# Performance work log

Hardware: AMD Instinct MI355X
Metric: run time of the kernel (lower is better)

## Reference

```python
import jax, jax.numpy as jnp
import numpy as np


def setup_inputs() -> dict:
    key = jax.random.key(0)
    ks = jax.random.split(key, 12)
    B, C, H, W = 8, 512, 48, 48
    HW = H * W
    inp = {
        'key': jax.random.normal(ks[0], (B, C, H, W), dtype=jnp.float32),
        'sds': jax.random.uniform(ks[1], (B, HW, H, W), dtype=jnp.float32),
        'global_bg': jax.random.normal(ks[2], (B, HW, C), dtype=jnp.float32),
        'global_fg': jax.random.normal(ks[3], (B, HW, C), dtype=jnp.float32),
        'local_bg': jax.random.normal(ks[4], (B, HW, C), dtype=jnp.float32),
        'local_fg': jax.random.normal(ks[5], (B, HW, C), dtype=jnp.float32),
        'overall_bg': jax.random.normal(ks[6], (B, 1, C), dtype=jnp.float32),
        'overall_fg': jax.random.normal(ks[7], (B, 1, C), dtype=jnp.float32),
        'short_bg': jax.random.normal(ks[8], (B, 1, C), dtype=jnp.float32),
        'short_fg': jax.random.normal(ks[9], (B, 1, C), dtype=jnp.float32),
        'long_bg': jax.random.normal(ks[10], (B, 1, C), dtype=jnp.float32),
        'long_fg': jax.random.normal(ks[11], (B, 1, C), dtype=jnp.float32),
    }
    return inp


def reference(key, sds, global_bg, global_fg, local_bg, local_fg,
              overall_bg, overall_fg, short_bg, short_fg, long_bg, long_fg):
    B, C, H, W = key.shape
    HW = H * W
    k = key.reshape(B, C, HW)                 # [B, C, HW]
    mask = sds.reshape(B, HW, HW)             # [B, HW(mem), HW(query)]

    def fine_max(bank, m=None):
        # bank: [B, HW, C]; score: [B, HW(mem), HW(query)]
        s = jnp.einsum('bmc,bcn->bmn', bank, k)
        if m is not None:
            s = s * m
        return jnp.max(s, axis=1).reshape(B, 1, H, W)

    def coarse(bank):
        # bank: [B, 1, C]
        return jnp.einsum('boc,bcn->bon', bank, k).reshape(B, 1, H, W)

    global_score = jnp.concatenate([fine_max(global_bg), fine_max(global_fg)], axis=1)
    local_score = jnp.concatenate([fine_max(local_bg, mask), fine_max(local_fg, mask)], axis=1)
    fine_score = jnp.concatenate([global_score, local_score], axis=1)

    coarse_score = jnp.concatenate([
        coarse(overall_bg), coarse(overall_fg),
        coarse(short_bg), coarse(short_fg),
        coarse(long_bg), coarse(long_fg),
    ], axis=1)

    matching_score = jnp.concatenate([fine_score, coarse_score], axis=1)  # [B, 10, H, W]
    return matching_score
```

## Files before the change

### kernel.cpp

```cpp
#include <hip/hip_runtime.h>

#define B_   8
#define C_   512
#define HW_  2304
#define BM   128
#define BN   128
#define BKQ  32
#define NKS  (C_ / BKQ)
#define NT_  (HW_ / BN)
#define MT_PER_BLOCK 3
#define MCHUNKS 6

typedef __bf16 bf16x8 __attribute__((ext_vector_type(8)));
typedef float  f32x4  __attribute__((ext_vector_type(4)));

__device__ __forceinline__ unsigned short f2bf(float f) {
  unsigned int u = __float_as_uint(f);
  u += 0x7FFF + ((u >> 16) & 1);
  return (unsigned short)(u >> 16);
}

__device__ __forceinline__ void gload_lds16(const void* g, void* l) {
  __builtin_amdgcn_global_load_lds(
      (const __attribute__((address_space(1))) unsigned int*)g,
      (__attribute__((address_space(3))) unsigned int*)l, 16, 0, 0);
}

__global__ void zero_out(float* __restrict__ out, int n) {
  int i = blockIdx.x * 256 + threadIdx.x;
  if (i < n) out[i] = 0.0f;
}

__global__ void transpose_coarse(const float* __restrict__ key,
                                 const float* __restrict__ v0, const float* __restrict__ v1,
                                 const float* __restrict__ v2, const float* __restrict__ v3,
                                 const float* __restrict__ v4, const float* __restrict__ v5,
                                 unsigned short* __restrict__ keyT,
                                 float* __restrict__ out) {
  __shared__ float tile[32][33];
  __shared__ float red2[6][8][32];
  int b  = blockIdx.z;
  int n0 = blockIdx.x * 32;
  int c0 = blockIdx.y * 32;
  int tx = threadIdx.x;
  int ty = threadIdx.y;
#pragma unroll
  for (int i = 0; i < 4; i++) {
    int c = c0 + ty + i * 8;
    tile[ty + i * 8][tx] = key[(size_t)b * C_ * HW_ + (size_t)c * HW_ + n0 + tx];
  }
  __syncthreads();
#pragma unroll
  for (int i = 0; i < 4; i++) {
    int n = n0 + ty + i * 8;
    keyT[(size_t)b * HW_ * C_ + (size_t)n * C_ + c0 + tx] = f2bf(tile[tx][ty + i * 8]);
  }
  float s[6] = {0.f, 0.f, 0.f, 0.f, 0.f, 0.f};
#pragma unroll
  for (int i = 0; i < 4; i++) {
    int cr = ty * 4 + i;
    int c  = c0 + cr;
    float kv = tile[cr][tx];
    s[0] += v0[b * C_ + c] * kv;
    s[1] += v1[b * C_ + c] * kv;
    s[2] += v2[b * C_ + c] * kv;
    s[3] += v3[b * C_ + c] * kv;
    s[4] += v4[b * C_ + c] * kv;
    s[5] += v5[b * C_ + c] * kv;
  }
#pragma unroll
  for (int j = 0; j < 6; j++) red2[j][ty][tx] = s[j];
  __syncthreads();
  if (ty < 6) {
    float a = 0.f;
#pragma unroll
    for (int k = 0; k < 8; k++) a += red2[ty][k][tx];
    atomicAdd(&out[((size_t)b * 10 + 4 + ty) * HW_ + n0 + tx], a);
  }
}

__global__ void convert_banks(const float* __restrict__ b0, const float* __restrict__ b1,
                              const float* __restrict__ b2, const float* __restrict__ b3,
                              unsigned short* __restrict__ out) {
  const size_t per = (size_t)B_ * HW_ * C_;
  int g = blockIdx.y;
  const float* src = (g == 0) ? b0 : (g == 1) ? b1 : (g == 2) ? b2 : b3;
  size_t i = ((size_t)blockIdx.x * blockDim.x + threadIdx.x) * 4;
  float4 v = *(const float4*)(src + i);
  ushort4 o;
  o.x = f2bf(v.x); o.y = f2bf(v.y); o.z = f2bf(v.z); o.w = f2bf(v.w);
  *(ushort4*)(out + g * per + i) = o;
}

__global__ __launch_bounds__(256, 3) void fine_kernel(
    const unsigned short* __restrict__ keyT,
    const unsigned short* __restrict__ banks,
    const float* __restrict__ sds,
    float* __restrict__ pmax) {
  int lin = blockIdx.x;
  int b   = lin & 7;
  int ix  = lin >> 3;
  int gp  = (ix >= 108) ? 1 : 0;
  int w   = ix - gp * 108;
  int mc  = w / NT_;
  int nt  = w % NT_;
  int n0  = nt * BN;

  __shared__ __align__(16) unsigned short sbuf[2][3][BM * BKQ];
  __shared__ float red[4 * BN];

  int t    = threadIdx.x;
  int wave = t >> 6;
  int lane = t & 63;
  int quad = lane >> 4;
  int l15  = lane & 15;
  int wm   = (wave & 1) * 64;
  int wn   = (wave >> 1) * 64;

  int ksub = (lane & 3) ^ ((lane >> 3) & 3);
  int swo  = (quad ^ ((l15 >> 1) & 3)) * 8;

  const unsigned short* bank0 = banks + ((size_t)(2 * gp) * B_ + b) * (size_t)HW_ * C_;
  const unsigned short* bank1 = banks + ((size_t)(2 * gp + 1) * B_ + b) * (size_t)HW_ * C_;
  const unsigned short* keyb  = keyT + (size_t)b * HW_ * C_;
  const float* maskb = sds + (size_t)b * HW_ * HW_;
  const bool masked = (gp == 1);

  auto STAGE = [&](int buf, int m0s, int kc) {
    unsigned short* A0d = &sbuf[buf][0][0];
    unsigned short* A1d = &sbuf[buf][1][0];
    unsigned short* Bd  = &sbuf[buf][2][0];
#pragma unroll
    for (int j = 0; j < 2; j++) {
      int rbase = j * 64 + wave * 16;
      size_t go = (size_t)(rbase + (lane >> 2)) * C_ + (size_t)kc * BKQ + ksub * 8;
      gload_lds16(bank0 + (size_t)m0s * C_ + go, &A0d[rbase * BKQ]);
      gload_lds16(bank1 + (size_t)m0s * C_ + go, &A1d[rbase * BKQ]);
      gload_lds16(keyb  + (size_t)n0  * C_ + go, &Bd [rbase * BKQ]);
    }
  };

  float rm0[4], rm1[4];
#pragma unroll
  for (int i = 0; i < 4; i++) { rm0[i] = -3.4e38f; rm1[i] = -3.4e38f; }

  int cur = 0;
  STAGE(0, mc * MT_PER_BLOCK * BM, 0);

  for (int mi = 0; mi < MT_PER_BLOCK; mi++) {
    int m0 = (mc * MT_PER_BLOCK + mi) * BM;
    f32x4 acc0[4][4], acc1[4][4];
#pragma unroll
    for (int i = 0; i < 4; i++)
#pragma unroll
      for (int j = 0; j < 4; j++)
#pragma unroll
        for (int e = 0; e < 4; e++) { acc0[i][j][e] = 0.0f; acc1[i][j][e] = 0.0f; }

    for (int kc = 0; kc < NKS; kc++) {
      __syncthreads();
      if (kc + 1 < NKS)                STAGE(cur ^ 1, m0, kc + 1);
      else if (mi + 1 < MT_PER_BLOCK)  STAGE(cur ^ 1, m0 + BM, 0);

      const unsigned short* A0s = &sbuf[cur][0][0];
      const unsigned short* A1s = &sbuf[cur][1][0];
      const unsigned short* Bs  = &sbuf[cur][2][0];
      bf16x8 a0[4], a1[4], bb[4];
#pragma unroll
      for (int ms = 0; ms < 4; ms++) {
        a0[ms] = *(const bf16x8*)(&A0s[(wm + ms * 16 + l15) * BKQ + swo]);
        a1[ms] = *(const bf16x8*)(&A1s[(wm + ms * 16 + l15) * BKQ + swo]);
      }
#pragma unroll
      for (int ns = 0; ns < 4; ns++)
        bb[ns] = *(const bf16x8*)(&Bs[(wn + ns * 16 + l15) * BKQ + swo]);
#pragma unroll
      for (int ms = 0; ms < 4; ms++)
#pragma unroll
        for (int ns = 0; ns < 4; ns++) {
          acc0[ms][ns] = __builtin_amdgcn_mfma_f32_16x16x32_bf16(
              a0[ms], bb[ns], acc0[ms][ns], 0, 0, 0);
          acc1[ms][ns] = __builtin_amdgcn_mfma_f32_16x16x32_bf16(
              a1[ms], bb[ns], acc1[ms][ns], 0, 0, 0);
        }
      cur ^= 1;
    }

#pragma unroll
    for (int ms = 0; ms < 4; ms++) {
#pragma unroll
      for (int ns = 0; ns < 4; ns++) {
        int n = n0 + wn + ns * 16 + l15;
#pragma unroll
        for (int r = 0; r < 4; r++) {
          int m = m0 + wm + ms * 16 + quad * 4 + r;
          float s0 = acc0[ms][ns][r];
          float s1 = acc1[ms][ns][r];
          if (masked) {
            float w_ = maskb[(size_t)m * HW_ + n];
            s0 *= w_; s1 *= w_;
          }
          rm0[ns] = fmaxf(rm0[ns], s0);
          rm1[ns] = fmaxf(rm1[ns], s1);
        }
      }
    }
  }

#pragma unroll
  for (int ns = 0; ns < 4; ns++) {
    float v = rm0[ns];
    v = fmaxf(v, __shfl_xor(v, 16, 64));
    v = fmaxf(v, __shfl_xor(v, 32, 64));
    rm0[ns] = v;
    float u = rm1[ns];
    u = fmaxf(u, __shfl_xor(u, 16, 64));
    u = fmaxf(u, __shfl_xor(u, 32, 64));
    rm1[ns] = u;
  }
  if (lane < 16) {
#pragma unroll
    for (int ns = 0; ns < 4; ns++) {
      red[(wave & 1) * BN + wn + ns * 16 + l15]           = rm0[ns];
      red[2 * BN + (wave & 1) * BN + wn + ns * 16 + l15]  = rm1[ns];
    }
  }
  __syncthreads();
  if (t < BN) {
    float vv0 = fmaxf(red[t], red[BN + t]);
    float vv1 = fmaxf(red[2 * BN + t], red[3 * BN + t]);
    pmax[(((size_t)mc * B_ + b) * 4 + 2 * gp)     * HW_ + n0 + t] = vv0;
    pmax[(((size_t)mc * B_ + b) * 4 + 2 * gp + 1) * HW_ + n0 + t] = vv1;
  }
}

__global__ void fine_combine(const float* __restrict__ pmax, float* __restrict__ out) {
  int i = blockIdx.x * 256 + threadIdx.x;
  if (i >= B_ * 4 * HW_) return;
  int n = i % HW_;
  int g = (i / HW_) % 4;
  int b = i / (HW_ * 4);
  float v = -3.4e38f;
#pragma unroll
  for (int mc = 0; mc < MCHUNKS; mc++)
    v = fmaxf(v, pmax[(((size_t)mc * B_ + b) * 4 + g) * HW_ + n]);
  out[((size_t)b * 10 + g) * HW_ + n] = v;
}

extern "C" void kernel_launch(void* const* d_in, const int* in_sizes, int n_in,
                              void* d_out, int out_size, void* d_ws, size_t ws_size,
                              hipStream_t stream) {
  const float* key  = (const float*)d_in[0];
  const float* sds  = (const float*)d_in[1];
  const float* gbg  = (const float*)d_in[2];
  const float* gfg  = (const float*)d_in[3];
  const float* lbg  = (const float*)d_in[4];
  const float* lfg  = (const float*)d_in[5];
  const float* obg  = (const float*)d_in[6];
  const float* ofg  = (const float*)d_in[7];
  const float* sbg  = (const float*)d_in[8];
  const float* sfg  = (const float*)d_in[9];
  const float* lobg = (const float*)d_in[10];
  const float* lofg = (const float*)d_in[11];
  float* out = (float*)d_out;

  unsigned short* keyT  = (unsigned short*)d_ws;
  unsigned short* banks = keyT + (size_t)B_ * HW_ * C_;
  float* pmax = (float*)(banks + (size_t)4 * B_ * HW_ * C_);

  zero_out<<<(out_size + 255) / 256, 256, 0, stream>>>(out, out_size);
  convert_banks<<<dim3((B_ * HW_ * C_) / (4 * 256), 4), 256, 0, stream>>>(gbg, gfg, lbg, lfg, banks);
  transpose_coarse<<<dim3(HW_ / 32, C_ / 32, B_), dim3(32, 8), 0, stream>>>(
      key, obg, ofg, sbg, sfg, lobg, lofg, keyT, out);
  fine_kernel<<<dim3(NT_ * MCHUNKS * 2 * B_), 256, 0, stream>>>(keyT, banks, sds, pmax);
  fine_combine<<<(B_ * 4 * HW_ + 255) / 256, 256, 0, stream>>>(pmax, out);
}
```

Before: 734.2 us.

## Deepen global-to-LDS prefetch to two stages with explicit waitcnt and barriers

```diff
diff --git a/kernel.cpp b/kernel.cpp
--- a/kernel.cpp
+++ b/kernel.cpp
@@ -10,6 +10,7 @@
 #define NT_  (HW_ / BN)
 #define MT_PER_BLOCK 3
 #define MCHUNKS 6
+#define NSTEPS (MT_PER_BLOCK * NKS)
 
 typedef __bf16 bf16x8 __attribute__((ext_vector_type(8)));
 typedef float  f32x4  __attribute__((ext_vector_type(4)));
@@ -126,10 +127,13 @@
   const float* maskb = sds + (size_t)b * HW_ * HW_;
   const bool masked = (gp == 1);
 
-  auto STAGE = [&](int buf, int m0s, int kc) {
-    unsigned short* A0d = &sbuf[buf][0][0];
-    unsigned short* A1d = &sbuf[buf][1][0];
-    unsigned short* Bd  = &sbuf[buf][2][0];
+  auto STAGE = [&](int P, int s) {
+    int mi  = s >> 4;
+    int kc  = s & 15;
+    int m0s = (mc * MT_PER_BLOCK + mi) * BM;
+    unsigned short* A0d = &sbuf[P][0][0];
+    unsigned short* A1d = &sbuf[P][1][0];
+    unsigned short* Bd  = &sbuf[P][2][0];
 #pragma unroll
     for (int j = 0; j < 2; j++) {
       int rbase = j * 64 + wave * 16;
@@ -144,48 +148,58 @@
 #pragma unroll
   for (int i = 0; i < 4; i++) { rm0[i] = -3.4e38f; rm1[i] = -3.4e38f; }
 
-  int cur = 0;
-  STAGE(0, mc * MT_PER_BLOCK * BM, 0);
+  f32x4 acc0[4][4], acc1[4][4];
+
+#define KSTEP(P, MI, KC)                                                       \
+  do {                                                                         \
+    int s_ = (MI) * 16 + (KC);                                                 \
+    if (s_ < NSTEPS - 2) asm volatile("s_waitcnt vmcnt(6)" ::: "memory");      \
+    else                 asm volatile("s_waitcnt vmcnt(0)" ::: "memory");      \
+    __builtin_amdgcn_s_barrier();                     \
+    __builtin_amdgcn_sched_barrier(0);                                         \
+    const unsigned short* A0s = &sbuf[P][0][0];                                \
+    const unsigned short* A1s = &sbuf[P][1][0];                                \
+    const unsigned short* Bs  = &sbuf[P][2][0];                                \
+    bf16x8 a0[4], a1[4], bb[4];                                                \
+    _Pragma("unroll") for (int ms = 0; ms < 4; ms++) {                         \
+      a0[ms] = *(const bf16x8*)(&A0s[(wm + ms * 16 + l15) * BKQ + swo]);       \
+      a1[ms] = *(const bf16x8*)(&A1s[(wm + ms * 16 + l15) * BKQ + swo]);       \
+    }                                                                          \
+    _Pragma("unroll") for (int ns = 0; ns < 4; ns++)                           \
+      bb[ns] = *(const bf16x8*)(&Bs[(wn + ns * 16 + l15) * BKQ + swo]);        \
+    asm volatile("s_waitcnt lgkmcnt(0)" ::: "memory");                         \
+    __builtin_amdgcn_sched_barrier(0);                                         \
+    __builtin_amdgcn_s_barrier();                \
+    __builtin_amdgcn_sched_barrier(0);                                         \
+    if (s_ + 2 < NSTEPS) STAGE(P, s_ + 2);       \
+    __builtin_amdgcn_s_setprio(1);                                             \
+    _Pragma("unroll") for (int ms = 0; ms < 4; ms++)                           \
+      _Pragma("unroll") for (int ns = 0; ns < 4; ns++) {                       \
+        acc0[ms][ns] = __builtin_amdgcn_mfma_f32_16x16x32_bf16(                \
+            a0[ms], bb[ns], acc0[ms][ns], 0, 0, 0);                            \
+        acc1[ms][ns] = __builtin_amdgcn_mfma_f32_16x16x32_bf16(                \
+            a1[ms], bb[ns], acc1[ms][ns], 0, 0, 0);                            \
+      }                                                                        \
+    __builtin_amdgcn_s_setprio(0);                                             \
+  } while (0)
+
+  STAGE(0, 0);
+  STAGE(1, 1);
 
   for (int mi = 0; mi < MT_PER_BLOCK; mi++) {
+#pragma unroll
+    for (int i = 0; i < 4; i++)
+#pragma unroll
+      for (int j = 0; j < 4; j++)
+#pragma unroll
+        for (int e = 0; e < 4; e++) { acc0[i][j][e] = 0.0f; acc1[i][j][e] = 0.0f; }
+
+    for (int kc2 = 0; kc2 < NKS; kc2 += 2) {
+      KSTEP(0, mi, kc2);
+      KSTEP(1, mi, kc2 + 1);
+    }
+
     int m0 = (mc * MT_PER_BLOCK + mi) * BM;
-    f32x4 acc0[4][4], acc1[4][4];
-#pragma unroll
-    for (int i = 0; i < 4; i++)
-#pragma unroll
-      for (int j = 0; j < 4; j++)
-#pragma unroll
-        for (int e = 0; e < 4; e++) { acc0[i][j][e] = 0.0f; acc1[i][j][e] = 0.0f; }
-
-    for (int kc = 0; kc < NKS; kc++) {
-      __syncthreads();
-      if (kc + 1 < NKS)                STAGE(cur ^ 1, m0, kc + 1);
-      else if (mi + 1 < MT_PER_BLOCK)  STAGE(cur ^ 1, m0 + BM, 0);
-
-      const unsigned short* A0s = &sbuf[cur][0][0];
-      const unsigned short* A1s = &sbuf[cur][1][0];
-      const unsigned short* Bs  = &sbuf[cur][2][0];
-      bf16x8 a0[4], a1[4], bb[4];
-#pragma unroll
-      for (int ms = 0; ms < 4; ms++) {
-        a0[ms] = *(const bf16x8*)(&A0s[(wm + ms * 16 + l15) * BKQ + swo]);
-        a1[ms] = *(const bf16x8*)(&A1s[(wm + ms * 16 + l15) * BKQ + swo]);
-      }
-#pragma unroll
-      for (int ns = 0; ns < 4; ns++)
-        bb[ns] = *(const bf16x8*)(&Bs[(wn + ns * 16 + l15) * BKQ + swo]);
-#pragma unroll
-      for (int ms = 0; ms < 4; ms++)
-#pragma unroll
-        for (int ns = 0; ns < 4; ns++) {
-          acc0[ms][ns] = __builtin_amdgcn_mfma_f32_16x16x32_bf16(
-              a0[ms], bb[ns], acc0[ms][ns], 0, 0, 0);
-          acc1[ms][ns] = __builtin_amdgcn_mfma_f32_16x16x32_bf16(
-              a1[ms], bb[ns], acc1[ms][ns], 0, 0, 0);
-        }
-      cur ^= 1;
-    }
-
 #pragma unroll
     for (int ms = 0; ms < 4; ms++) {
 #pragma unroll
@@ -206,6 +220,7 @@
       }
     }
   }
+#undef KSTEP
 
 #pragma unroll
   for (int ns = 0; ns < 4; ns++) {
```

New measurement: 1.165 ms. +58.6%, slower.

## Split fine GEMM across 8 waves with triple-buffered LDS pipeline

Applied to the files above, without the earlier changes.

```diff
diff --git a/kernel.cpp b/kernel.cpp
--- a/kernel.cpp
+++ b/kernel.cpp
@@ -10,6 +10,9 @@
 #define NT_  (HW_ / BN)
 #define MT_PER_BLOCK 3
 #define MCHUNKS 6
+#define NSTEPS (MT_PER_BLOCK * NKS)
+#define TILE_SH (BM * BKQ)
+#define BUF_SH  (3 * TILE_SH)
 
 typedef __bf16 bf16x8 __attribute__((ext_vector_type(8)));
 typedef float  f32x4  __attribute__((ext_vector_type(4)));
@@ -92,7 +95,7 @@
   *(ushort4*)(out + g * per + i) = o;
 }
 
-__global__ __launch_bounds__(256, 3) void fine_kernel(
+__global__ __launch_bounds__(512, 4) void fine_kernel(
     const unsigned short* __restrict__ keyT,
     const unsigned short* __restrict__ banks,
     const float* __restrict__ sds,
@@ -106,19 +109,21 @@
   int nt  = w % NT_;
   int n0  = nt * BN;
 
-  __shared__ __align__(16) unsigned short sbuf[2][3][BM * BKQ];
-  __shared__ float red[4 * BN];
+  __shared__ __align__(16) unsigned short sbuf[3][3][TILE_SH];
+  __shared__ float red[8][64];
 
   int t    = threadIdx.x;
   int wave = t >> 6;
   int lane = t & 63;
   int quad = lane >> 4;
   int l15  = lane & 15;
-  int wm   = (wave & 1) * 64;
-  int wn   = (wave >> 1) * 64;
-
-  int ksub = (lane & 3) ^ ((lane >> 3) & 3);
-  int swo  = (quad ^ ((l15 >> 1) & 3)) * 8;
+  int bank_i = wave & 1;
+  int wm   = ((wave >> 1) & 1) * 64;
+  int wn   = (wave >> 2) * 64;
+
+  int rbase = wave * 16;
+  int ksub  = (lane & 3) ^ ((lane >> 3) & 3);
+  int swo   = (quad ^ ((l15 >> 1) & 3)) * 8;
 
   const unsigned short* bank0 = banks + ((size_t)(2 * gp) * B_ + b) * (size_t)HW_ * C_;
   const unsigned short* bank1 = banks + ((size_t)(2 * gp + 1) * B_ + b) * (size_t)HW_ * C_;
@@ -126,66 +131,65 @@
   const float* maskb = sds + (size_t)b * HW_ * HW_;
   const bool masked = (gp == 1);
 
-  auto STAGE = [&](int buf, int m0s, int kc) {
-    unsigned short* A0d = &sbuf[buf][0][0];
-    unsigned short* A1d = &sbuf[buf][1][0];
-    unsigned short* Bd  = &sbuf[buf][2][0];
-#pragma unroll
-    for (int j = 0; j < 2; j++) {
-      int rbase = j * 64 + wave * 16;
-      size_t go = (size_t)(rbase + (lane >> 2)) * C_ + (size_t)kc * BKQ + ksub * 8;
-      gload_lds16(bank0 + (size_t)m0s * C_ + go, &A0d[rbase * BKQ]);
-      gload_lds16(bank1 + (size_t)m0s * C_ + go, &A1d[rbase * BKQ]);
-      gload_lds16(keyb  + (size_t)n0  * C_ + go, &Bd [rbase * BKQ]);
+  auto STAGE = [&](int P, int s) {
+    int mi  = s >> 4;
+    int kc  = s & 15;
+    size_t m0s = (size_t)(mc * MT_PER_BLOCK + mi) * BM;
+    unsigned short* dst = &sbuf[0][0][0] + P * BUF_SH + rbase * BKQ;
+    size_t go = (size_t)(rbase + (lane >> 2)) * C_ + (size_t)kc * BKQ + ksub * 8;
+    gload_lds16(bank0 + m0s * C_ + go, dst);
+    gload_lds16(bank1 + m0s * C_ + go, dst + TILE_SH);
+    gload_lds16(keyb + (size_t)n0 * C_ + go, dst + 2 * TILE_SH);
+  };
+
+  float rm[4];
+#pragma unroll
+  for (int i = 0; i < 4; i++) rm[i] = -3.4e38f;
+
+  STAGE(0, 0);
+  STAGE(1, 1);
+
+  for (int mi = 0; mi < MT_PER_BLOCK; mi++) {
+    f32x4 acc[4][4];
+#pragma unroll
+    for (int i = 0; i < 4; i++)
+#pragma unroll
+      for (int j = 0; j < 4; j++)
+#pragma unroll
+        for (int e = 0; e < 4; e++) acc[i][j][e] = 0.0f;
+
+    for (int kc = 0; kc < NKS; kc++) {
+      int s = (mi << 4) | kc;
+      if (s < NSTEPS - 1) asm volatile("s_waitcnt vmcnt(3)" ::: "memory");
+      else                asm volatile("s_waitcnt vmcnt(0)" ::: "memory");
+      __builtin_amdgcn_s_barrier();
+      int sn = s + 2;
+      if (sn < NSTEPS) STAGE(sn % 3, sn);
+
+      const unsigned short* base  = &sbuf[0][0][0] + (s % 3) * BUF_SH;
+      const unsigned short* Abase = base + bank_i * TILE_SH;
+      const unsigned short* Bbase = base + 2 * TILE_SH;
+      bf16x8 a[4], bv[4];
+#pragma unroll
+      for (int ms = 0; ms < 4; ms++)
+        a[ms] = *(const bf16x8*)(Abase + (wm + ms * 16 + l15) * BKQ + swo);
+#pragma unroll
+      for (int ns = 0; ns < 4; ns++)
+        bv[ns] = *(const bf16x8*)(Bbase + (wn + ns * 16 + l15) * BKQ + swo);
+      asm volatile("s_waitcnt lgkmcnt(0)" ::: "memory");
+      __builtin_amdgcn_sched_barrier(0);
+
+      __builtin_amdgcn_s_setprio(1);
+#pragma unroll
+      for (int ms = 0; ms < 4; ms++)
+#pragma unroll
+        for (int ns = 0; ns < 4; ns++)
+          acc[ms][ns] = __builtin_amdgcn_mfma_f32_16x16x32_bf16(
+              a[ms], bv[ns], acc[ms][ns], 0, 0, 0);
+      __builtin_amdgcn_s_setprio(0);
     }
-  };
-
-  float rm0[4], rm1[4];
-#pragma unroll
-  for (int i = 0; i < 4; i++) { rm0[i] = -3.4e38f; rm1[i] = -3.4e38f; }
-
-  int cur = 0;
-  STAGE(0, mc * MT_PER_BLOCK * BM, 0);
-
-  for (int mi = 0; mi < MT_PER_BLOCK; mi++) {
+
     int m0 = (mc * MT_PER_BLOCK + mi) * BM;
-    f32x4 acc0[4][4], acc1[4][4];
-#pragma unroll
-    for (int i = 0; i < 4; i++)
-#pragma unroll
-      for (int j = 0; j < 4; j++)
-#pragma unroll
-        for (int e = 0; e < 4; e++) { acc0[i][j][e] = 0.0f; acc1[i][j][e] = 0.0f; }
-
-    for (int kc = 0; kc < NKS; kc++) {
-      __syncthreads();
-      if (kc + 1 < NKS)                STAGE(cur ^ 1, m0, kc + 1);
-      else if (mi + 1 < MT_PER_BLOCK)  STAGE(cur ^ 1, m0 + BM, 0);
-
-      const unsigned short* A0s = &sbuf[cur][0][0];
-      const unsigned short* A1s = &sbuf[cur][1][0];
-      const unsigned short* Bs  = &sbuf[cur][2][0];
-      bf16x8 a0[4], a1[4], bb[4];
-#pragma unroll
-      for (int ms = 0; ms < 4; ms++) {
-        a0[ms] = *(const bf16x8*)(&A0s[(wm + ms * 16 + l15) * BKQ + swo]);
-        a1[ms] = *(const bf16x8*)(&A1s[(wm + ms * 16 + l15) * BKQ + swo]);
-      }
-#pragma unroll
-      for (int ns = 0; ns < 4; ns++)
-        bb[ns] = *(const bf16x8*)(&Bs[(wn + ns * 16 + l15) * BKQ + swo]);
-#pragma unroll
-      for (int ms = 0; ms < 4; ms++)
-#pragma unroll
-        for (int ns = 0; ns < 4; ns++) {
-          acc0[ms][ns] = __builtin_amdgcn_mfma_f32_16x16x32_bf16(
-              a0[ms], bb[ns], acc0[ms][ns], 0, 0, 0);
-          acc1[ms][ns] = __builtin_amdgcn_mfma_f32_16x16x32_bf16(
-              a1[ms], bb[ns], acc1[ms][ns], 0, 0, 0);
-        }
-      cur ^= 1;
-    }
-
 #pragma unroll
     for (int ms = 0; ms < 4; ms++) {
 #pragma unroll
@@ -194,14 +198,12 @@
 #pragma unroll
         for (int r = 0; r < 4; r++) {
           int m = m0 + wm + ms * 16 + quad * 4 + r;
-          float s0 = acc0[ms][ns][r];
-          float s1 = acc1[ms][ns][r];
+          float s0 = acc[ms][ns][r];
           if (masked) {
             float w_ = maskb[(size_t)m * HW_ + n];
-            s0 *= w_; s1 *= w_;
+            s0 *= w_;
           }
-          rm0[ns] = fmaxf(rm0[ns], s0);
-          rm1[ns] = fmaxf(rm1[ns], s1);
+          rm[ns] = fmaxf(rm[ns], s0);
         }
       }
     }
@@ -209,28 +211,23 @@
 
 #pragma unroll
   for (int ns = 0; ns < 4; ns++) {
-    float v = rm0[ns];
+    float v = rm[ns];
     v = fmaxf(v, __shfl_xor(v, 16, 64));
     v = fmaxf(v, __shfl_xor(v, 32, 64));
-    rm0[ns] = v;
-    float u = rm1[ns];
-    u = fmaxf(u, __shfl_xor(u, 16, 64));
-    u = fmaxf(u, __shfl_xor(u, 32, 64));
-    rm1[ns] = u;
+    rm[ns] = v;
   }
   if (lane < 16) {
 #pragma unroll
-    for (int ns = 0; ns < 4; ns++) {
-      red[(wave & 1) * BN + wn + ns * 16 + l15]           = rm0[ns];
-      red[2 * BN + (wave & 1) * BN + wn + ns * 16 + l15]  = rm1[ns];
-    }
+    for (int ns = 0; ns < 4; ns++) red[wave][ns * 16 + l15] = rm[ns];
   }
   __syncthreads();
-  if (t < BN) {
-    float vv0 = fmaxf(red[t], red[BN + t]);
-    float vv1 = fmaxf(red[2 * BN + t], red[3 * BN + t]);
-    pmax[(((size_t)mc * B_ + b) * 4 + 2 * gp)     * HW_ + n0 + t] = vv0;
-    pmax[(((size_t)mc * B_ + b) * 4 + 2 * gp + 1) * HW_ + n0 + t] = vv1;
+  if (t < 256) {
+    int bank = t >> 7;
+    int nn   = t & 127;
+    int wnh  = nn >> 6;
+    int nl   = nn & 63;
+    float v = fmaxf(red[bank + wnh * 4][nl], red[bank + 2 + wnh * 4][nl]);
+    pmax[(((size_t)mc * B_ + b) * 4 + 2 * gp + bank) * HW_ + n0 + nn] = v;
   }
 }
 
@@ -272,6 +269,6 @@
   convert_banks<<<dim3((B_ * HW_ * C_) / (4 * 256), 4), 256, 0, stream>>>(gbg, gfg, lbg, lfg, banks);
   transpose_coarse<<<dim3(HW_ / 32, C_ / 32, B_), dim3(32, 8), 0, stream>>>(
       key, obg, ofg, sbg, sfg, lobg, lofg, keyT, out);
-  fine_kernel<<<dim3(NT_ * MCHUNKS * 2 * B_), 256, 0, stream>>>(keyT, banks, sds, pmax);
+  fine_kernel<<<dim3(NT_ * MCHUNKS * 2 * B_), 512, 0, stream>>>(keyT, banks, sds, pmax);
   fine_combine<<<(B_ * 4 * HW_ + 255) / 256, 256, 0, stream>>>(pmax, out);
 }
```

After: 851.4 us. 1.16x slower.
